# Optimization experiments

Measured on AMD Instinct MI355X. Metric: run time of the kernel, lower is better.

## Reference

```python
import jax, jax.numpy as jnp
import numpy as np
from jax import lax

B, H, W = 64, 40, 40
K = 24        # num_capsules == num_templates
TS = 11       # template_size
F = 16        # num_feature_maps
PI = 3.141592653589793


def setup_inputs() -> dict:
    key = jax.random.key(0)
    ks = jax.random.split(key, 12)
    def nrm(k, shape, s):
        return jax.random.normal(k, shape, dtype=jnp.float32) * s
    inp = {"x": jax.random.normal(ks[0], (B, 1, H, W), dtype=jnp.float32)}
    wshapes = [(K, 128, 1, 3, 3), (K, 128, 128, 3, 3), (K, 128, 128, 3, 3), (K, 128, 128, 3, 3), (K, F, 128, 1, 1)]
    for i, sh in enumerate(wshapes):
        fan_in = sh[2] * sh[3] * sh[4]
        inp["w%d" % (i + 1)] = nrm(ks[1 + i], sh, (2.0 / fan_in) ** 0.5)
        inp["b%d" % (i + 1)] = nrm(ks[6 + i], (K, sh[1]), 0.1)
    inp["templates"] = jax.random.normal(ks[11], (K, TS, TS), dtype=jnp.float32)
    return inp


def _capsule(x, w1, b1, w2, b2, w3, b3, w4, b4, w5, b5):
    # one part-capsule conv stack; x: [B,1,H,W]
    def cv(h, w, b, s):
        y = lax.conv_general_dilated(h, w, (s, s), 'VALID', dimension_numbers=('NCHW', 'OIHW', 'NCHW'))
        return y + b[None, :, None, None]
    h = jax.nn.relu(cv(x, w1, b1, 2))
    h = jax.nn.relu(cv(h, w2, b2, 2))
    h = jax.nn.relu(cv(h, w3, b3, 1))
    h = jax.nn.relu(cv(h, w4, b4, 1))
    return cv(h, w5, b5, 1)  # [B,F,5,5]


def _warp(templates, pose, Ho, Wo):
    # Batched replacement for the per-sample PIL affine + resize round-trip.
    # templates: [T,TS,TS]; pose: [B,T,6] = (angle_deg, tx, ty, scale, shear_x_deg, shear_y_deg)
    T_ = templates.shape[0]
    ang = jnp.deg2rad(pose[..., 0])
    tx, ty = pose[..., 1], pose[..., 2]
    sc = jnp.maximum(pose[..., 3], 1e-2)  # guard against scale==0 from ReLU
    shx = jnp.deg2rad(pose[..., 4])
    shy = jnp.deg2rad(pose[..., 5])
    cx = cy = (TS - 1) * 0.5
    # torchvision _get_inverse_affine_matrix
    a = jnp.cos(ang - shy) / jnp.cos(shy)
    b = -jnp.cos(ang - shy) * jnp.tan(shx) / jnp.cos(shy) - jnp.sin(ang)
    c = jnp.sin(ang - shy) / jnp.cos(shy)
    d = -jnp.sin(ang - shy) * jnp.tan(shx) / jnp.cos(shy) + jnp.cos(ang)
    m0 = d / sc; m1 = -b / sc; m3 = -c / sc; m4 = a / sc
    m2 = m0 * (-cx - tx) + m1 * (-cy - ty) + cx
    m5 = m3 * (-cx - tx) + m4 * (-cy - ty) + cy
    # output grid in template pixel coords (fuses the bilinear resize TS->HoxWo)
    gy = (jnp.arange(Ho, dtype=jnp.float32) + 0.5) * TS / Ho - 0.5
    gx = (jnp.arange(Wo, dtype=jnp.float32) + 0.5) * TS / Wo - 0.5
    yo, xo = jnp.meshgrid(gy, gx, indexing='ij')  # [Ho,Wo]
    xin = m0[..., None, None] * xo + m1[..., None, None] * yo + m2[..., None, None]  # [B,T,Ho,Wo]
    yin = m3[..., None, None] * xo + m4[..., None, None] * yo + m5[..., None, None]
    x0 = jnp.floor(xin); y0 = jnp.floor(yin)
    wx = xin - x0; wy = yin - y0
    x0i = x0.astype(jnp.int32); y0i = y0.astype(jnp.int32)
    tidx = jnp.arange(T_)[None, :, None, None]
    def tap(yi, xi):
        valid = (xi >= 0) & (xi < TS) & (yi >= 0) & (yi < TS)
        v = templates[tidx, jnp.clip(yi, 0, TS - 1), jnp.clip(xi, 0, TS - 1)]
        return jnp.where(valid, v, 0.0)
    return (tap(y0i, x0i) * (1 - wx) * (1 - wy) + tap(y0i, x0i + 1) * wx * (1 - wy)
            + tap(y0i + 1, x0i) * (1 - wx) * wy + tap(y0i + 1, x0i + 1) * wx * wy)


def reference(x, w1, b1, w2, b2, w3, b3, w4, b4, w5, b5, templates):
    out = jax.vmap(_capsule, in_axes=(None,) + (0,) * 10)(x, w1, b1, w2, b2, w3, b3, w4, b4, w5, b5)  # [K,B,F,5,5]
    # torch Softmax(2) on [B,Hc,Wc] attention map = softmax over each row (last axis)
    att = jax.nn.softmax(out[:, :, -1], axis=-1)                       # [K,B,5,5]
    pooled = jnp.sum(out[:, :, :-1] * att[:, :, None], axis=(-2, -1))  # [K,B,F-1]
    p = pooled.transpose(1, 0, 2)                                      # [B,K,F-1]
    x_m = jax.nn.relu(p[:, :, :6])
    d_m = jax.nn.sigmoid(p[:, :, 6:7])
    c_z = jax.nn.relu(p[:, :, 7:])
    Bn = x.shape[0]
    # PIL round-trip in the original detaches gradients from templates/poses
    tt = lax.stop_gradient(_warp(templates, x_m, H, W))                # [B,K,H,W]
    mix = jax.nn.softmax(d_m * tt.reshape(Bn, K, -1), axis=-1).reshape(Bn, K, H, W)
    std = jnp.std(x.reshape(Bn, -1), axis=-1, ddof=1).reshape(Bn, 1, 1, 1)
    mult = 1.0 / jnp.sqrt(std * 2.0 * PI)
    pw = -1.0 / (2.0 * std * std)
    g = mult * jnp.exp((lax.stop_gradient(x) - tt) ** 2 * pw)          # [B,K,H,W]
    ll = jnp.mean(jnp.sum(jnp.log(jnp.sum(g * mix, axis=1)), axis=(-2, -1)))
    tflat = jnp.broadcast_to(lax.stop_gradient(templates).reshape(1, K, TS * TS), (Bn, K, TS * TS))
    input_ocae = jnp.concatenate([lax.stop_gradient(d_m), lax.stop_gradient(x_m), tflat, c_z], axis=-1)
    return ll, input_ocae, lax.stop_gradient(x_m), lax.stop_gradient(d_m)
```

## Files before the change

kernel.cpp:

```cpp
#include <hip/hip_runtime.h>
#include <math.h>

#define TPB 256

typedef __attribute__((ext_vector_type(8))) short s16x8;
typedef __attribute__((ext_vector_type(4))) short s16x4;
typedef __attribute__((ext_vector_type(4))) float f32x4;
typedef unsigned int u32;

constexpr int Bn = 64, Kc = 24, TSz = 11;
constexpr int NBK = Bn * Kc;

constexpr size_t SZW_B    = (size_t)Kc * 36 * 4096 * 2;
constexpr size_t OFFB_W2  = 0;
constexpr size_t OFFB_W3  = OFFB_W2 + SZW_B;
constexpr size_t OFFB_W4  = OFFB_W3 + SZW_B;
constexpr size_t OFFB_DMV = OFFB_W4 + SZW_B;
constexpr size_t OFFB_TT  = OFFB_DMV + (size_t)NBK * 4;
constexpr size_t OFFB_ST  = OFFB_TT + (size_t)NBK * 1600 * 4;
constexpr size_t OFFB_MXS = OFFB_ST + 512;
constexpr size_t OFFB_PART= OFFB_MXS + (size_t)NBK * 2 * 4;

constexpr int OUT_OC = 1;
constexpr int OUT_XM = 1 + NBK * 136;
constexpr int OUT_DM = OUT_XM + NBK * 6;

__device__ __forceinline__ ushort f2b(float f) {
    union { float f; unsigned u; } c; c.f = f;
    unsigned r = c.u + 0x7fffu + ((c.u >> 16) & 1u);
    return (ushort)(r >> 16);
}
__device__ __forceinline__ float b2f(ushort h) {
    union { unsigned u; float f; } c; c.u = ((unsigned)h) << 16; return c.f;
}

__device__ __forceinline__ float blockReduceSum(float v) {
    __shared__ float red[4];
    __syncthreads();
#pragma unroll
    for (int o = 32; o > 0; o >>= 1) v += __shfl_down(v, o, 64);
    int lane = threadIdx.x & 63, wv = threadIdx.x >> 6;
    if (lane == 0) red[wv] = v;
    __syncthreads();
    return red[0] + red[1] + red[2] + red[3];
}

__device__ __forceinline__ float blockReduceSum512(float v) {
    __shared__ float red8[8];
    __syncthreads();
#pragma unroll
    for (int o = 32; o > 0; o >>= 1) v += __shfl_down(v, o, 64);
    int lane = threadIdx.x & 63, wv = threadIdx.x >> 6;
    if (lane == 0) red8[wv] = v;
    __syncthreads();
    float s = 0.f;
#pragma unroll
    for (int i = 0; i < 8; ++i) s += red8[i];
    return s;
}

__device__ __forceinline__ float blockReduceMax512(float v) {
    __shared__ float redm8[8];
    __syncthreads();
#pragma unroll
    for (int o = 32; o > 0; o >>= 1) v = fmaxf(v, __shfl_down(v, o, 64));
    int lane = threadIdx.x & 63, wv = threadIdx.x >> 6;
    if (lane == 0) redm8[wv] = v;
    __syncthreads();
    float m = redm8[0];
#pragma unroll
    for (int i = 1; i < 8; ++i) m = fmaxf(m, redm8[i]);
    return m;
}

__global__ __launch_bounds__(TPB) void prep_k(
    const float* __restrict__ w2, const float* __restrict__ w3,
    const float* __restrict__ w4, const float* __restrict__ x,
    ushort* __restrict__ wt2, ushort* __restrict__ wt3,
    ushort* __restrict__ wt4, float* __restrict__ st) {
    const int bid = blockIdx.x;
    if (bid < 9216) {
        __shared__ float ld[1152];
        const float* w = bid < 3072 ? w2 : (bid < 6144 ? w3 : w4);
        ushort* wt = bid < 3072 ? wt2 : (bid < 6144 ? wt3 : wt4);
        const int kk = (bid % 3072) >> 7, cout = bid & 127;
        const float* src = w + (size_t)(kk * 128 + cout) * 1152;
        for (int i = threadIdx.x; i < 1152; i += TPB) ld[i] = src[i];
        __syncthreads();
        const int n = cout >> 4, l16 = cout & 15;
        for (int e = threadIdx.x; e < 1152; e += TPB) {
            int cb = e / 288, r = e - cb * 288, tap = r >> 5, c32 = r & 31;
            int cin = cb * 32 + c32;
            size_t d = (size_t)((kk * 4 + cb) * 9 + tap) * 4096
                     + n * 512 + (c32 >> 3) * 128 + l16 * 8 + (c32 & 7);
            wt[d] = f2b(ld[cin * 9 + tap]);
        }
    } else {
        const int b = bid - 9216;
        const float* xb = x + b * 1600;
        float s = 0.f, s2 = 0.f;
        for (int p = threadIdx.x; p < 1600; p += TPB) {
            float v = xb[p];
            s += v; s2 += v * v;
        }
        s = blockReduceSum(s);
        s2 = blockReduceSum(s2);
        if (threadIdx.x == 0) {
            float mean = s / 1600.f;
            float var = (s2 - 1600.f * mean * mean) / 1599.f;
            float sd = sqrtf(var);
            st[b * 2] = rsqrtf(sd * 6.283185307179586f);
            st[b * 2 + 1] = -1.f / (2.f * sd * sd);
        }
    }
}

__global__ __launch_bounds__(512) void convall_k(
    const float* __restrict__ x, const float* __restrict__ w1,
    const float* __restrict__ b1,
    const ushort* __restrict__ wt2, const float* __restrict__ b2,
    const ushort* __restrict__ wt3, const float* __restrict__ b3,
    const ushort* __restrict__ wt4, const float* __restrict__ b4,
    const float* __restrict__ w5, const float* __restrict__ b5,
    const float* __restrict__ tpl,
    float* __restrict__ dmv, float* __restrict__ tt,
    float* __restrict__ mxs, float* __restrict__ out) {
    __shared__ __align__(16) ushort pool[17680];
    float*  xs  = (float*)pool;
    ushort* As  = pool + 3200;
    ushort* h2L = pool;
    ushort* h3L = pool + 11016;
    float*  h4s = (float*)pool;
    float*  outs= (float*)(pool + 6400);
    float*  atts= (float*)(pool + 7200);
    float*  pooled = (float*)(pool + 7264);
    float*  tp  = (float*)(pool + 7400);

    const int bi = blockIdx.x;
    const int xcd = bi & 7, jj = bi >> 3;
    const int k = xcd * 3 + jj % 3, b = jj / 3;
    const int bkL = b * 24 + k;
    const int tid = threadIdx.x;
    const int w = tid >> 6, l = tid & 63, l16 = l & 15, g = l >> 4;
    const int mgrp = w >> 2, ngrp = w & 3;

    {
        constexpr int OP = 81, STR = 40;
        const int sl = tid & 7, p0 = tid >> 3;
        const ushort* wb = wt2 + (size_t)k * 36 * 4096 + ngrp * 1024 + g * 128 + l16 * 8;
        const float* w1k = w1 + (size_t)k * 1152;
        const float* b1k = b1 + k * 128;

        for (int i = tid; i < 400; i += 512)
            ((f32x4*)xs)[i] = ((const f32x4*)(x + b * 1600))[i];

        f32x4 acc[3][2];
#pragma unroll
        for (int m = 0; m < 3; ++m)
#pragma unroll
            for (int n = 0; n < 2; ++n) acc[m][n] = (f32x4)0.f;

        int ibase[3];
#pragma unroll
        for (int m = 0; m < 3; ++m) {
            int row = (mgrp * 3 + m) * 16 + l16;
            row = row < OP ? row : OP - 1;
            int oy = row / 9, ox = row - oy * 9;
            ibase[m] = oy * 38 + ox * 2;
        }

        auto conv1_slab = [&](int cb) {
            float wq[36], bq[4];
            const float* wsrc = w1k + (cb * 32 + sl * 4) * 9;
#pragma unroll
            for (int i2 = 0; i2 < 9; ++i2) ((f32x4*)wq)[i2] = ((const f32x4*)wsrc)[i2];
            *(f32x4*)bq = *(const f32x4*)(b1k + cb * 32 + sl * 4);
#pragma unroll
            for (int jp = 0; jp < 6; ++jp) {
                int p = p0 + jp * 64;
                if (p < 361) {
                    int py = p / 19, px = p - py * 19;
                    const float* xb = xs + py * 80 + px * 2;
                    float xt[9];
#pragma unroll
                    for (int dy = 0; dy < 3; ++dy)
#pragma unroll
                        for (int dx = 0; dx < 3; ++dx) xt[dy * 3 + dx] = xb[dy * 40 + dx];
                    s16x4 v;
#pragma unroll
                    for (int j2 = 0; j2 < 4; ++j2) {
                        float s2 = bq[j2];
#pragma unroll
                        for (int t9 = 0; t9 < 9; ++t9) s2 += wq[j2 * 9 + t9] * xt[t9];
                        v[j2] = (short)f2b(fmaxf(s2, 0.f));
                    }
                    *(s16x4*)(As + p * STR + 8 * ((sl >> 1) ^ ((p >> 3) & 1)) + (sl & 1) * 4) = v;
                }
            }
        };

        s16x8 breg[2][2];
        __syncthreads();
        conv1_slab(0);
#pragma unroll
        for (int n = 0; n < 2; ++n) breg[0][n] = *(const s16x8*)(wb + n * 512);
        __syncthreads();

#pragma unroll
        for (int cb = 0; cb < 4; ++cb) {
#pragma unroll
            for (int tap = 0; tap < 9; ++tap) {
                const int it = cb * 9 + tap;
                if (tap < 8) {
                    const ushort* src = wb + (size_t)(it + 1) * 4096;
#pragma unroll
                    for (int n = 0; n < 2; ++n)
                        breg[(it + 1) & 1][n] = *(const s16x8*)(src + n * 512);
                }
                const int ioff = (tap / 3) * 19 + (tap % 3);
                s16x8 a[3];
#pragma unroll
                for (int m = 0; m < 3; ++m) {
                    int ip = ibase[m] + ioff;
                    a[m] = *(const s16x8*)(As + ip * STR + 8 * (g ^ ((ip >> 3) & 1)));
                }
#pragma unroll
                for (int n = 0; n < 2; ++n)
#pragma unroll
                    for (int m = 0; m < 3; ++m)
                        acc[m][n] = __builtin_amdgcn_mfma_f32_16x16x32_bf16(a[m], breg[it & 1][n], acc[m][n], 0, 0, 0);
            }
            if (cb < 3) {
                __syncthreads();
                conv1_slab(cb + 1);
                const ushort* src = wb + (size_t)((cb + 1) * 9) * 4096;
#pragma unroll
                for (int n = 0; n < 2; ++n)
                    breg[((cb + 1) * 9) & 1][n] = *(const s16x8*)(src + n * 512);
                __syncthreads();
            }
        }
        __syncthreads();
#pragma unroll
        for (int n = 0; n < 2; ++n) {
            int cout = (ngrp * 2 + n) * 16 + l16;
            float bv = b2[k * 128 + cout];
#pragma unroll
            for (int m = 0; m < 3; ++m)
#pragma unroll
                for (int r = 0; r < 4; ++r) {
                    int row = (mgrp * 3 + m) * 16 + g * 4 + r;
                    if (row < OP)
                        h2L[row * 136 + cout] = f2b(fmaxf(acc[m][n][r] + bv, 0.f));
                }
        }
    }
    __syncthreads();

    {
        constexpr int OP = 49;
        const ushort* wb = wt3 + (size_t)k * 36 * 4096 + ngrp * 1024 + g * 128 + l16 * 8;
        s16x8 breg[2][2];
#pragma unroll
        for (int n = 0; n < 2; ++n) breg[0][n] = *(const s16x8*)(wb + n * 512);
#pragma unroll
        for (int n = 0; n < 2; ++n) breg[1][n] = *(const s16x8*)(wb + 4096 + n * 512);

        f32x4 acc[2][2];
#pragma unroll
        for (int m = 0; m < 2; ++m)
#pragma unroll
            for (int n = 0; n < 2; ++n) acc[m][n] = (f32x4)0.f;

        int ibase[2];
#pragma unroll
        for (int m = 0; m < 2; ++m) {
            int row = (mgrp * 2 + m) * 16 + l16;
            row = row < OP ? row : OP - 1;
            int oy = row / 7, ox = row - oy * 7;
            ibase[m] = oy * 9 + ox;
        }
#pragma unroll
        for (int cb = 0; cb < 4; ++cb)
#pragma unroll
            for (int tap = 0; tap < 9; ++tap) {
                const int it = cb * 9 + tap;
                if (it + 1 < 36) {
                    const ushort* src = wb + (size_t)(it + 1) * 4096;
#pragma unroll
                    for (int n = 0; n < 2; ++n)
                        breg[(it + 1) & 1][n] = *(const s16x8*)(src + n * 512);
                }
                const int ioff = (tap / 3) * 9 + (tap % 3);
                s16x8 a[2];
#pragma unroll
                for (int m = 0; m < 2; ++m)
                    a[m] = *(const s16x8*)(h2L + (ibase[m] + ioff) * 136 + cb * 32 + g * 8);
#pragma unroll
                for (int n = 0; n < 2; ++n)
#pragma unroll
                    for (int m = 0; m < 2; ++m)
                        acc[m][n] = __builtin_amdgcn_mfma_f32_16x16x32_bf16(a[m], breg[it & 1][n], acc[m][n], 0, 0, 0);
            }
#pragma unroll
        for (int n = 0; n < 2; ++n) {
            int cout = (ngrp * 2 + n) * 16 + l16;
            float bv = b3[k * 128 + cout];
#pragma unroll
            for (int m = 0; m < 2; ++m)
#pragma unroll
                for (int r = 0; r < 4; ++r) {
                    int row = (mgrp * 2 + m) * 16 + g * 4 + r;
                    if (row < OP)
                        h3L[row * 136 + cout] = f2b(fmaxf(acc[m][n][r] + bv, 0.f));
                }
        }
    }
    __syncthreads();

    {
        constexpr int OP = 25;
        const ushort* wb = wt4 + (size_t)k * 36 * 4096 + ngrp * 1024 + g * 128 + l16 * 8;
        s16x8 breg[2][2];
#pragma unroll
        for (int n = 0; n < 2; ++n) breg[0][n] = *(const s16x8*)(wb + n * 512);
#pragma unroll
        for (int n = 0; n < 2; ++n) breg[1][n] = *(const s16x8*)(wb + 4096 + n * 512);

        f32x4 acc[2];
#pragma unroll
        for (int n = 0; n < 2; ++n) acc[n] = (f32x4)0.f;

        int ibase;
        {
            int row = mgrp * 16 + l16;
            row = row < OP ? row : OP - 1;
            int oy = row / 5, ox = row - oy * 5;
            ibase = oy * 7 + ox;
        }
#pragma unroll
        for (int cb = 0; cb < 4; ++cb)
#pragma unroll
            for (int tap = 0; tap < 9; ++tap) {
                const int it = cb * 9 + tap;
                if (it + 1 < 36) {
                    const ushort* src = wb + (size_t)(it + 1) * 4096;
#pragma unroll
                    for (int n = 0; n < 2; ++n)
                        breg[(it + 1) & 1][n] = *(const s16x8*)(src + n * 512);
                }
                const int ioff = (tap / 3) * 7 + (tap % 3);
                s16x8 a = *(const s16x8*)(h3L + (ibase + ioff) * 136 + cb * 32 + g * 8);
#pragma unroll
                for (int n = 0; n < 2; ++n)
                    acc[n] = __builtin_amdgcn_mfma_f32_16x16x32_bf16(a, breg[it & 1][n], acc[n], 0, 0, 0);
            }
#pragma unroll
        for (int n = 0; n < 2; ++n) {
            int cout = (ngrp * 2 + n) * 16 + l16;
            float bv = b4[k * 128 + cout];
#pragma unroll
            for (int r = 0; r < 4; ++r) {
                int row = mgrp * 16 + g * 4 + r;
                if (row < OP)
                    h4s[cout * 25 + row] = fmaxf(acc[n][r] + bv, 0.f);
            }
        }
    }
    __syncthreads();

    for (int t = tid; t < 400; t += 512) {
        int f = t / 25, pix = t - f * 25;
        const float* wp = w5 + (size_t)(k * 16 + f) * 128;
        float s = b5[k * 16 + f];
        for (int c = 0; c < 128; ++c) s += wp[c] * h4s[c * 25 + pix];
        outs[t] = s;
    }
    __syncthreads();
    if (tid < 25) {
        int y5 = tid / 5;
        const float* row = outs + 15 * 25 + y5 * 5;
        float mx = row[0];
#pragma unroll
        for (int j = 1; j < 5; ++j) mx = fmaxf(mx, row[j]);
        float ssum = 0.f;
#pragma unroll
        for (int j = 0; j < 5; ++j) ssum += expf(row[j] - mx);
        atts[tid] = expf(outs[15 * 25 + tid] - mx) / ssum;
    }
    __syncthreads();
    if (tid < 15) {
        float s = 0.f;
        const float* row = outs + tid * 25;
#pragma unroll
        for (int p = 0; p < 25; ++p) s += row[p] * atts[p];
        pooled[tid] = s;
    }
    __syncthreads();
    float* oc = out + OUT_OC + (size_t)bkL * 136;
    if (tid < 6) {
        float v = fmaxf(pooled[tid], 0.f);
        oc[1 + tid] = v;
        out[OUT_XM + bkL * 6 + tid] = v;
    } else if (tid == 6) {
        float d = 1.f / (1.f + expf(-pooled[6]));
        dmv[bkL] = d;
        oc[0] = d;
        out[OUT_DM + bkL] = d;
    } else if (tid >= 7 && tid < 15) {
        oc[128 + tid - 7] = fmaxf(pooled[tid], 0.f);
    }
    for (int t = tid; t < 121; t += 512) oc[7 + t] = tpl[k * 121 + t];

    for (int i = tid; i < 121; i += 512) tp[i] = tpl[k * 121 + i];
    {
        const float D2R = 0.017453292519943295f;
        float ang = fmaxf(pooled[0], 0.f) * D2R;
        float txp = fmaxf(pooled[1], 0.f), typ = fmaxf(pooled[2], 0.f);
        float sc  = fmaxf(fmaxf(pooled[3], 0.f), 1e-2f);
        float shx = fmaxf(pooled[4], 0.f) * D2R;
        float shy = fmaxf(pooled[5], 0.f) * D2R;
        float dm  = 1.f / (1.f + expf(-pooled[6]));
        float cams = cosf(ang - shy), sams = sinf(ang - shy);
        float cshy = cosf(shy), tshx = tanf(shx);
        float av = cams / cshy;
        float bv = -cams * tshx / cshy - sinf(ang);
        float cv = sams / cshy;
        float dv = -sams * tshx / cshy + cosf(ang);
        float m0 = dv / sc, m1 = -bv / sc, m3 = -cv / sc, m4 = av / sc;
        float m2 = m0 * (-5.f - txp) + m1 * (-5.f - typ) + 5.f;
        float m5 = m3 * (-5.f - txp) + m4 * (-5.f - typ) + 5.f;
        __syncthreads();
        float* to = tt + (size_t)bkL * 1600;
        float tvl[4];
#pragma unroll
        for (int r = 0; r < 4; ++r) {
            int p = tid + r * 512;
            float val = 0.f;
            if (p < 1600) {
                int i = p / 40, jx = p - (p / 40) * 40;
                float gx = (jx + 0.5f) * (11.f / 40.f) - 0.5f;
                float gy = (i + 0.5f) * (11.f / 40.f) - 0.5f;
                float xin = m0 * gx + m1 * gy + m2;
                float yin = m3 * gx + m4 * gy + m5;
                float x0 = floorf(xin), y0 = floorf(yin);
                float wx = xin - x0, wy = yin - y0;
                int x0i = (int)x0, y0i = (int)y0;
                auto tapf = [&](int yy, int xx) -> float {
                    bool valid = (xx >= 0) && (xx < TSz) && (yy >= 0) && (yy < TSz);
                    int yc = min(max(yy, 0), TSz - 1), xc = min(max(xx, 0), TSz - 1);
                    float v = tp[yc * TSz + xc];
                    return valid ? v : 0.f;
                };
                float v00 = tapf(y0i, x0i),     v01 = tapf(y0i, x0i + 1);
                float v10 = tapf(y0i + 1, x0i), v11 = tapf(y0i + 1, x0i + 1);
                val = v00 * (1.f - wx) * (1.f - wy) + v01 * wx * (1.f - wy) +
                      v10 * (1.f - wx) * wy + v11 * wx * wy;
                to[p] = val;
            }
            tvl[r] = val;
        }
        float mx = -1e30f;
#pragma unroll
        for (int r = 0; r < 4; ++r) {
            int p = tid + r * 512;
            if (p < 1600) mx = fmaxf(mx, dm * tvl[r]);
        }
        mx = blockReduceMax512(mx);
        float s = 0.f;
#pragma unroll
        for (int r = 0; r < 4; ++r) {
            int p = tid + r * 512;
            if (p < 1600) s += expf(dm * tvl[r] - mx);
        }
        s = blockReduceSum512(s);
        if (tid == 0) { mxs[bkL * 2] = mx; mxs[bkL * 2 + 1] = s; }
    }
}

__global__ __launch_bounds__(TPB) void ll_k(const float* __restrict__ x,
                                            const float* __restrict__ tt,
                                            const float* __restrict__ dmv,
                                            const float* __restrict__ mxs,
                                            const float* __restrict__ st,
                                            float* __restrict__ part) {
    const int b = blockIdx.x, sp = blockIdx.y;
    __shared__ float dms[24], mxh[24], sih[24];
    if (threadIdx.x < 24) {
        int bk = b * 24 + threadIdx.x;
        dms[threadIdx.x] = dmv[bk];
        mxh[threadIdx.x] = mxs[bk * 2];
        sih[threadIdx.x] = 1.f / mxs[bk * 2 + 1];
    }
    __syncthreads();
    const float mult = st[b * 2], pw = st[b * 2 + 1];
    const float* xb = x + b * 1600;
    const float* tb = tt + (size_t)b * 24 * 1600;
    float acc = 0.f;
    int p = sp * 200 + threadIdx.x;
    if (threadIdx.x < 200) {
        float xv = xb[p];
        float ssum = 0.f;
        for (int k = 0; k < 24; ++k) {
            float tv = tb[(size_t)k * 1600 + p];
            float dd = xv - tv;
            float g = mult * expf(dd * dd * pw);
            float mixv = expf(dms[k] * tv - mxh[k]) * sih[k];
            ssum += g * mixv;
        }
        acc = logf(ssum);
    }
    acc = blockReduceSum(acc);
    if (threadIdx.x == 0) part[b * 8 + sp] = acc;
}

__global__ void fin_k(const float* __restrict__ part, float* __restrict__ out) {
    float v = 0.f;
#pragma unroll
    for (int q = 0; q < 8; ++q) v += part[threadIdx.x * 8 + q];
#pragma unroll
    for (int o = 32; o > 0; o >>= 1) v += __shfl_down(v, o, 64);
    if (threadIdx.x == 0) out[0] = v * (1.f / 64.f);
}

extern "C" void kernel_launch(void* const* d_in, const int* in_sizes, int n_in,
                              void* d_out, int out_size, void* d_ws, size_t ws_size,
                              hipStream_t stream) {
    const float* x   = (const float*)d_in[0];
    const float* w1  = (const float*)d_in[1];
    const float* b1  = (const float*)d_in[2];
    const float* w2  = (const float*)d_in[3];
    const float* b2  = (const float*)d_in[4];
    const float* w3  = (const float*)d_in[5];
    const float* b3  = (const float*)d_in[6];
    const float* w4  = (const float*)d_in[7];
    const float* b4  = (const float*)d_in[8];
    const float* w5  = (const float*)d_in[9];
    const float* b5  = (const float*)d_in[10];
    const float* tpl = (const float*)d_in[11];
    float* out = (float*)d_out;
    char* W = (char*)d_ws;

    ushort* wt2 = (ushort*)(W + OFFB_W2);
    ushort* wt3 = (ushort*)(W + OFFB_W3);
    ushort* wt4 = (ushort*)(W + OFFB_W4);
    float*  dmv  = (float*)(W + OFFB_DMV);
    float*  ttb  = (float*)(W + OFFB_TT);
    float*  stv  = (float*)(W + OFFB_ST);
    float*  mxs  = (float*)(W + OFFB_MXS);
    float*  part = (float*)(W + OFFB_PART);

    prep_k<<<3 * 3072 + Bn, TPB, 0, stream>>>(w2, w3, w4, x, wt2, wt3, wt4, stv);
    convall_k<<<NBK, 512, 0, stream>>>(x, w1, b1, wt2, b2, wt3, b3, wt4, b4,
                                       w5, b5, tpl, dmv, ttb, mxs, out);
    ll_k<<<dim3(Bn, 8), TPB, 0, stream>>>(x, ttb, dmv, mxs, stv, part);
    fin_k<<<1, 64, 0, stream>>>(part, out);
}
```

Measured before the change: 227.5 us.

## Warp-specialize conv2: producer waves compute conv1 slabs into double-buffered LDS

Splits the 8 waves of the conv2 stage into 4 consumer waves, each issuing twice as many MFMAs over the full 128 output channels, and 4 producer waves that compute the next conv1 input slab into a second LDS buffer. This is meant to overlap the scalar conv1 work with the matrix work. Conv3 and conv4 switch to a three-deep weight register prefetch and stop unrolling the channel-block loop. In exchange, LDS use grows to about 64 KB, which may lower occupancy, and only half the waves do MFMA during conv2.

```diff
diff --git a/kernel.cpp b/kernel.cpp
--- a/kernel.cpp
+++ b/kernel.cpp
@@ -125,9 +125,10 @@
     const float* __restrict__ tpl,
     float* __restrict__ dmv, float* __restrict__ tt,
     float* __restrict__ mxs, float* __restrict__ out) {
-    __shared__ __align__(16) ushort pool[17680];
+    __shared__ __align__(16) ushort pool[32080];
     float*  xs  = (float*)pool;
-    ushort* As  = pool + 3200;
+    ushort* As0 = pool + 3200;
+    ushort* As1 = pool + 17640;
     ushort* h2L = pool;
     ushort* h3L = pool + 11016;
     float*  h4s = (float*)pool;
@@ -142,23 +143,24 @@
     const int bkL = b * 24 + k;
     const int tid = threadIdx.x;
     const int w = tid >> 6, l = tid & 63, l16 = l & 15, g = l >> 4;
-    const int mgrp = w >> 2, ngrp = w & 3;
 
     {
         constexpr int OP = 81, STR = 40;
-        const int sl = tid & 7, p0 = tid >> 3;
-        const ushort* wb = wt2 + (size_t)k * 36 * 4096 + ngrp * 1024 + g * 128 + l16 * 8;
+        const int mgrp = (w >> 1) & 1, ngrp = w & 1;
+        const int tid2 = tid & 255;
+        const int sl = tid2 & 7, p0 = tid2 >> 3;
+        const ushort* wb = wt2 + (size_t)k * 36 * 4096 + ngrp * 2048 + g * 128 + l16 * 8;
         const float* w1k = w1 + (size_t)k * 1152;
         const float* b1k = b1 + k * 128;
 
         for (int i = tid; i < 400; i += 512)
             ((f32x4*)xs)[i] = ((const f32x4*)(x + b * 1600))[i];
 
-        f32x4 acc[3][2];
+        f32x4 acc[3][4];
 #pragma unroll
         for (int m = 0; m < 3; ++m)
 #pragma unroll
-            for (int n = 0; n < 2; ++n) acc[m][n] = (f32x4)0.f;
+            for (int n = 0; n < 4; ++n) acc[m][n] = (f32x4)0.f;
 
         int ibase[3];
 #pragma unroll
@@ -169,98 +171,99 @@
             ibase[m] = oy * 38 + ox * 2;
         }
 
-        auto conv1_slab = [&](int cb) {
+        auto conv1_slab = [&](int cb, ushort* dA) {
             float wq[36], bq[4];
             const float* wsrc = w1k + (cb * 32 + sl * 4) * 9;
 #pragma unroll
             for (int i2 = 0; i2 < 9; ++i2) ((f32x4*)wq)[i2] = ((const f32x4*)wsrc)[i2];
             *(f32x4*)bq = *(const f32x4*)(b1k + cb * 32 + sl * 4);
-#pragma unroll
-            for (int jp = 0; jp < 6; ++jp) {
-                int p = p0 + jp * 64;
-                if (p < 361) {
-                    int py = p / 19, px = p - py * 19;
-                    const float* xb = xs + py * 80 + px * 2;
-                    float xt[9];
-#pragma unroll
-                    for (int dy = 0; dy < 3; ++dy)
-#pragma unroll
-                        for (int dx = 0; dx < 3; ++dx) xt[dy * 3 + dx] = xb[dy * 40 + dx];
-                    s16x4 v;
-#pragma unroll
-                    for (int j2 = 0; j2 < 4; ++j2) {
-                        float s2 = bq[j2];
-#pragma unroll
-                        for (int t9 = 0; t9 < 9; ++t9) s2 += wq[j2 * 9 + t9] * xt[t9];
-                        v[j2] = (short)f2b(fmaxf(s2, 0.f));
+            for (int p = p0; p < 361; p += 32) {
+                int py = p / 19, px = p - py * 19;
+                const float* xb = xs + py * 80 + px * 2;
+                float xt[9];
+#pragma unroll
+                for (int dy = 0; dy < 3; ++dy)
+#pragma unroll
+                    for (int dx = 0; dx < 3; ++dx) xt[dy * 3 + dx] = xb[dy * 40 + dx];
+                s16x4 v;
+#pragma unroll
+                for (int j2 = 0; j2 < 4; ++j2) {
+                    float s2 = bq[j2];
+#pragma unroll
+                    for (int t9 = 0; t9 < 9; ++t9) s2 += wq[j2 * 9 + t9] * xt[t9];
+                    v[j2] = (short)f2b(fmaxf(s2, 0.f));
+                }
+                *(s16x4*)(dA + p * STR + 8 * ((sl >> 1) ^ ((p >> 3) & 1)) + (sl & 1) * 4) = v;
+            }
+        };
+
+        s16x8 breg[3][4];
+        __syncthreads();
+        if (w >= 4) {
+            conv1_slab(0, As0);
+        } else {
+#pragma unroll
+            for (int n = 0; n < 4; ++n) breg[0][n] = *(const s16x8*)(wb + n * 512);
+#pragma unroll
+            for (int n = 0; n < 4; ++n) breg[1][n] = *(const s16x8*)(wb + 4096 + n * 512);
+        }
+        __syncthreads();
+
+#pragma unroll 1
+        for (int cb = 0; cb < 4; ++cb) {
+            ushort* curA = (cb & 1) ? As1 : As0;
+            ushort* nxtA = (cb & 1) ? As0 : As1;
+            if (w >= 4) {
+                if (cb < 3) conv1_slab(cb + 1, nxtA);
+            } else {
+#pragma unroll
+                for (int tap = 0; tap < 9; ++tap) {
+                    const int it = cb * 9 + tap;
+                    if (it + 2 < 36) {
+                        const ushort* src = wb + (size_t)(it + 2) * 4096;
+#pragma unroll
+                        for (int n = 0; n < 4; ++n)
+                            breg[(tap + 2) % 3][n] = *(const s16x8*)(src + n * 512);
                     }
-                    *(s16x4*)(As + p * STR + 8 * ((sl >> 1) ^ ((p >> 3) & 1)) + (sl & 1) * 4) = v;
+                    const int ioff = (tap / 3) * 19 + (tap % 3);
+                    s16x8 a[3];
+#pragma unroll
+                    for (int m = 0; m < 3; ++m) {
+                        int ip = ibase[m] + ioff;
+                        a[m] = *(const s16x8*)(curA + ip * STR + 8 * (g ^ ((ip >> 3) & 1)));
+                    }
+#pragma unroll
+                    for (int n = 0; n < 4; ++n)
+#pragma unroll
+                        for (int m = 0; m < 3; ++m)
+                            acc[m][n] = __builtin_amdgcn_mfma_f32_16x16x32_bf16(a[m], breg[tap % 3][n], acc[m][n], 0, 0, 0);
                 }
             }
-        };
-
-        s16x8 breg[2][2];
-        __syncthreads();
-        conv1_slab(0);
-#pragma unroll
-        for (int n = 0; n < 2; ++n) breg[0][n] = *(const s16x8*)(wb + n * 512);
-        __syncthreads();
-
-#pragma unroll
-        for (int cb = 0; cb < 4; ++cb) {
-#pragma unroll
-            for (int tap = 0; tap < 9; ++tap) {
-                const int it = cb * 9 + tap;
-                if (tap < 8) {
-                    const ushort* src = wb + (size_t)(it + 1) * 4096;
-#pragma unroll
-                    for (int n = 0; n < 2; ++n)
-                        breg[(it + 1) & 1][n] = *(const s16x8*)(src + n * 512);
-                }
-                const int ioff = (tap / 3) * 19 + (tap % 3);
-                s16x8 a[3];
-#pragma unroll
-                for (int m = 0; m < 3; ++m) {
-                    int ip = ibase[m] + ioff;
-                    a[m] = *(const s16x8*)(As + ip * STR + 8 * (g ^ ((ip >> 3) & 1)));
-                }
-#pragma unroll
-                for (int n = 0; n < 2; ++n)
-#pragma unroll
-                    for (int m = 0; m < 3; ++m)
-                        acc[m][n] = __builtin_amdgcn_mfma_f32_16x16x32_bf16(a[m], breg[it & 1][n], acc[m][n], 0, 0, 0);
-            }
-            if (cb < 3) {
-                __syncthreads();
-                conv1_slab(cb + 1);
-                const ushort* src = wb + (size_t)((cb + 1) * 9) * 4096;
-#pragma unroll
-                for (int n = 0; n < 2; ++n)
-                    breg[((cb + 1) * 9) & 1][n] = *(const s16x8*)(src + n * 512);
-                __syncthreads();
-            }
-        }
-        __syncthreads();
-#pragma unroll
-        for (int n = 0; n < 2; ++n) {
-            int cout = (ngrp * 2 + n) * 16 + l16;
-            float bv = b2[k * 128 + cout];
-#pragma unroll
-            for (int m = 0; m < 3; ++m)
-#pragma unroll
-                for (int r = 0; r < 4; ++r) {
-                    int row = (mgrp * 3 + m) * 16 + g * 4 + r;
-                    if (row < OP)
-                        h2L[row * 136 + cout] = f2b(fmaxf(acc[m][n][r] + bv, 0.f));
-                }
+            __syncthreads();
+        }
+        if (w < 4) {
+#pragma unroll
+            for (int n = 0; n < 4; ++n) {
+                int cout = (ngrp * 4 + n) * 16 + l16;
+                float bv = b2[k * 128 + cout];
+#pragma unroll
+                for (int m = 0; m < 3; ++m)
+#pragma unroll
+                    for (int r = 0; r < 4; ++r) {
+                        int row = (mgrp * 3 + m) * 16 + g * 4 + r;
+                        if (row < OP)
+                            h2L[row * 136 + cout] = f2b(fmaxf(acc[m][n][r] + bv, 0.f));
+                    }
+            }
         }
     }
     __syncthreads();
 
     {
         constexpr int OP = 49;
-        const ushort* wb = wt3 + (size_t)k * 36 * 4096 + ngrp * 1024 + g * 128 + l16 * 8;
-        s16x8 breg[2][2];
+        const int mg = w >> 2, ng = w & 3;
+        const ushort* wb = wt3 + (size_t)k * 36 * 4096 + ng * 1024 + g * 128 + l16 * 8;
+        s16x8 breg[3][2];
 #pragma unroll
         for (int n = 0; n < 2; ++n) breg[0][n] = *(const s16x8*)(wb + n * 512);
 #pragma unroll
@@ -275,21 +278,21 @@
         int ibase[2];
 #pragma unroll
         for (int m = 0; m < 2; ++m) {
-            int row = (mgrp * 2 + m) * 16 + l16;
+            int row = (mg * 2 + m) * 16 + l16;
             row = row < OP ? row : OP - 1;
             int oy = row / 7, ox = row - oy * 7;
             ibase[m] = oy * 9 + ox;
         }
-#pragma unroll
+#pragma unroll 1
         for (int cb = 0; cb < 4; ++cb)
 #pragma unroll
             for (int tap = 0; tap < 9; ++tap) {
                 const int it = cb * 9 + tap;
-                if (it + 1 < 36) {
-                    const ushort* src = wb + (size_t)(it + 1) * 4096;
+                if (it + 2 < 36) {
+                    const ushort* src = wb + (size_t)(it + 2) * 4096;
 #pragma unroll
                     for (int n = 0; n < 2; ++n)
-                        breg[(it + 1) & 1][n] = *(const s16x8*)(src + n * 512);
+                        breg[(tap + 2) % 3][n] = *(const s16x8*)(src + n * 512);
                 }
                 const int ioff = (tap / 3) * 9 + (tap % 3);
                 s16x8 a[2];
@@ -300,17 +303,17 @@
                 for (int n = 0; n < 2; ++n)
 #pragma unroll
                     for (int m = 0; m < 2; ++m)
-                        acc[m][n] = __builtin_amdgcn_mfma_f32_16x16x32_bf16(a[m], breg[it & 1][n], acc[m][n], 0, 0, 0);
+                        acc[m][n] = __builtin_amdgcn_mfma_f32_16x16x32_bf16(a[m], breg[tap % 3][n], acc[m][n], 0, 0, 0);
             }
 #pragma unroll
         for (int n = 0; n < 2; ++n) {
-            int cout = (ngrp * 2 + n) * 16 + l16;
+            int cout = (ng * 2 + n) * 16 + l16;
             float bv = b3[k * 128 + cout];
 #pragma unroll
             for (int m = 0; m < 2; ++m)
 #pragma unroll
                 for (int r = 0; r < 4; ++r) {
-                    int row = (mgrp * 2 + m) * 16 + g * 4 + r;
+                    int row = (mg * 2 + m) * 16 + g * 4 + r;
                     if (row < OP)
                         h3L[row * 136 + cout] = f2b(fmaxf(acc[m][n][r] + bv, 0.f));
                 }
@@ -320,8 +323,9 @@
 
     {
         constexpr int OP = 25;
-        const ushort* wb = wt4 + (size_t)k * 36 * 4096 + ngrp * 1024 + g * 128 + l16 * 8;
-        s16x8 breg[2][2];
+        const int mg = w >> 2, ng = w & 3;
+        const ushort* wb = wt4 + (size_t)k * 36 * 4096 + ng * 1024 + g * 128 + l16 * 8;
+        s16x8 breg[3][2];
 #pragma unroll
         for (int n = 0; n < 2; ++n) breg[0][n] = *(const s16x8*)(wb + n * 512);
 #pragma unroll
@@ -333,35 +337,35 @@
 
         int ibase;
         {
-            int row = mgrp * 16 + l16;
+            int row = mg * 16 + l16;
             row = row < OP ? row : OP - 1;
             int oy = row / 5, ox = row - oy * 5;
             ibase = oy * 7 + ox;
         }
-#pragma unroll
+#pragma unroll 1
         for (int cb = 0; cb < 4; ++cb)
 #pragma unroll
             for (int tap = 0; tap < 9; ++tap) {
                 const int it = cb * 9 + tap;
-                if (it + 1 < 36) {
-                    const ushort* src = wb + (size_t)(it + 1) * 4096;
+                if (it + 2 < 36) {
+                    const ushort* src = wb + (size_t)(it + 2) * 4096;
 #pragma unroll
                     for (int n = 0; n < 2; ++n)
-                        breg[(it + 1) & 1][n] = *(const s16x8*)(src + n * 512);
+                        breg[(tap + 2) % 3][n] = *(const s16x8*)(src + n * 512);
                 }
                 const int ioff = (tap / 3) * 7 + (tap % 3);
                 s16x8 a = *(const s16x8*)(h3L + (ibase + ioff) * 136 + cb * 32 + g * 8);
 #pragma unroll
                 for (int n = 0; n < 2; ++n)
-                    acc[n] = __builtin_amdgcn_mfma_f32_16x16x32_bf16(a, breg[it & 1][n], acc[n], 0, 0, 0);
+                    acc[n] = __builtin_amdgcn_mfma_f32_16x16x32_bf16(a, breg[tap % 3][n], acc[n], 0, 0, 0);
             }
 #pragma unroll
         for (int n = 0; n < 2; ++n) {
-            int cout = (ngrp * 2 + n) * 16 + l16;
+            int cout = (ng * 2 + n) * 16 + l16;
             float bv = b4[k * 128 + cout];
 #pragma unroll
             for (int r = 0; r < 4; ++r) {
-                int row = mgrp * 16 + g * 4 + r;
+                int row = mg * 16 + g * 4 + r;
                 if (row < OP)
                     h4s[cout * 25 + row] = fmaxf(acc[n][r] + bv, 0.f);
             }
```

Measured after the change: 237.6 us. +4.4%, slower.
